# Kernel tuning notes

Measured on AMD Instinct MI355X. Metric: run time of the kernel, lower is better.

## Reference

```python
import jax, jax.numpy as jnp
import numpy as np

NEG = -10000.0
EPS = 1e-5

B, N, H, DEPTH = 4096, 64, 128, 3
H2 = H // 2


def setup_inputs() -> dict:
    key = jax.random.key(0)
    k1, k2, k3 = jax.random.split(key, 3)
    hidden_states = jax.random.normal(k1, (B, N, H), dtype=jnp.float32)
    li_vector_num = jax.random.randint(k2, (B,), 0, N + 1, dtype=jnp.int32)
    Ws = jax.random.normal(k3, (DEPTH, H, H2), dtype=jnp.float32) * (1.0 / np.sqrt(H))
    bs = jnp.zeros((DEPTH, H2), dtype=jnp.float32)
    ln_w = jnp.ones((DEPTH, H2), dtype=jnp.float32)
    ln_b = jnp.zeros((DEPTH, H2), dtype=jnp.float32)
    return {"hidden_states": hidden_states, "li_vector_num": li_vector_num,
            "Ws": Ws, "bs": bs, "ln_w": ln_w, "ln_b": ln_b}


def _subgraph(hidden_states, Ws, bs, ln_w, ln_b, li_vector_num):
    b, n, h = hidden_states.shape
    # padding mask: -10000 for invalid vectors (i >= li_vector_num), per polyline
    pad = jnp.where(jnp.arange(n)[None, :] >= li_vector_num[:, None], NEG, 0.0)
    pad = pad.astype(hidden_states.dtype)[:, :, None]  # [B,N,1]
    hs = hidden_states
    for l in range(Ws.shape[0]):
        # MLP: linear -> layernorm -> relu
        x = jnp.einsum('bnh,hk->bnk', hs, Ws[l]) + bs[l]
        mu = jnp.mean(x, axis=-1, keepdims=True)
        var = jnp.mean((x - mu) ** 2, axis=-1, keepdims=True)
        x = ln_w[l] * (x - mu) * jax.lax.rsqrt(var + EPS) + ln_b[l]
        enc = jax.nn.relu(x)  # [B,N,H2]
        m = enc + pad  # masked encoded states
        # leave-one-out max over vector dim via top-2 trick (replaces O(N^2) loop)
        top2 = jax.lax.top_k(jnp.swapaxes(m, 1, 2), 2)[0]  # [B,H2,2]
        top1b = top2[..., 0][:, None, :]  # [B,1,H2]
        top2b = top2[..., 1][:, None, :]  # [B,1,H2]
        loo = jnp.where(m == top1b, top2b, top1b)  # max over i != j
        loo = jnp.maximum(loo, m + NEG)            # faithful: j itself at -10000
        loo = jnp.maximum(loo, 0.0)                # torch.max(max_hidden, zeros)
        hs = jnp.concatenate([enc, loo], axis=-1)  # [B,N,H]
    return jnp.max(hs, axis=1)  # [B,H]


def reference(hidden_states, li_vector_num, Ws, bs, ln_w, ln_b):
    return _subgraph(hidden_states, Ws, bs, ln_w, ln_b, li_vector_num)
```

## Files before the change

### kernel.cpp

```cpp
#include <hip/hip_runtime.h>
#include <hip/hip_bf16.h>

#define NEGV (-10000.0f)
#define EPSV (1e-5f)
#define NINF (-3.4e38f)

typedef __attribute__((ext_vector_type(8))) short short8;
typedef __attribute__((ext_vector_type(4))) float floatx4;

constexpr int Bsz = 4096, Nv = 64, Hd = 128, DEPTH = 3, H2 = 64;
constexpr int HSTR = 136;

struct alignas(8) BH4 { __hip_bfloat162 a, b; };

__device__ __forceinline__ unsigned short f2b(float f) {
    unsigned int u = __builtin_bit_cast(unsigned int, f);
    u += 0x7fffu + ((u >> 16) & 1u);
    return (unsigned short)(u >> 16);
}

__device__ __forceinline__ void t2ins(float& t1, float& t2, float v) {
    float lo = fminf(t1, v); t1 = fmaxf(t1, v); t2 = fmaxf(t2, lo);
}
__device__ __forceinline__ void t2merge(float& t1, float& t2, float o1, float o2) {
    float lo = fminf(t1, o1); t1 = fmaxf(t1, o1); t2 = fmaxf(fmaxf(t2, o2), lo);
}

__global__ void prep_w(const float* __restrict__ Ws, unsigned short* __restrict__ wt) {
    int idx = blockIdx.x * 256 + threadIdx.x;
    if (idx < DEPTH * 8192) {
        int l = idx >> 13, o = idx & 8191;
        int j = o & 7, q = (o >> 3) & 63, hi = (o >> 9) & 3, kt = o >> 11;
        int k = kt * 32 + hi * 8 + j;
        int srccol = (q & 15) * 4 + (q >> 4);
        wt[idx] = f2b(Ws[l * 8192 + k * 64 + srccol]);
    }
}

__global__ __launch_bounds__(256, 4)
void subgraph_kernel(const float* __restrict__ hidden, const int* __restrict__ lvn,
                     const unsigned short* __restrict__ wt,
                     const float* __restrict__ bsv, const float* __restrict__ lnw,
                     const float* __restrict__ lnb, float* __restrict__ out)
{
    __shared__ __hip_bfloat16 hsb[Nv][HSTR];
    __shared__ float scbuf[4][128];

    const int b = blockIdx.x, t = threadIdx.x;
    const int L = lvn[b];
    const int lane = t & 63, wid = t >> 6;
    const int lr = lane & 15, hi = lane >> 4;
    const int arow = wid * 16 + lr;

    const float4* src = (const float4*)(hidden + (size_t)b * Nv * Hd);
#pragma unroll
    for (int i = 0; i < 8; ++i) {
        int idx4 = t + i * 256;
        float4 v = src[idx4];
        int flat = idx4 * 4, n = flat >> 7, h = flat & 127;
        BH4 pk;
        pk.a = __float22bfloat162_rn(make_float2(v.x, v.y));
        pk.b = __float22bfloat162_rn(make_float2(v.z, v.w));
        *(BH4*)&hsb[n][h] = pk;
    }

    float madd[4];
#pragma unroll
    for (int reg = 0; reg < 4; ++reg) {
        int row = wid * 16 + hi * 4 + reg;
        madd[reg] = (row >= L) ? NEGV : 0.0f;
    }
    __syncthreads();

    float encmax[4], loomax[4];

    for (int l = 0; l < DEPTH; ++l) {
        const unsigned short* wbase = wt + l * 8192;

        short8 af[4];
#pragma unroll
        for (int kt = 0; kt < 4; ++kt)
            af[kt] = *(const short8*)&hsb[arow][kt * 32 + hi * 8];

        floatx4 acc[4];
#pragma unroll
        for (int ct = 0; ct < 4; ++ct) { floatx4 z = {0.f, 0.f, 0.f, 0.f}; acc[ct] = z; }
#pragma unroll
        for (int kt = 0; kt < 4; ++kt)
#pragma unroll
            for (int ct = 0; ct < 4; ++ct) {
                short8 bf = *(const short8*)(wbase + ((kt * 4 + hi) * 64 + ct * 16 + lr) * 8);
                acc[ct] = __builtin_amdgcn_mfma_f32_16x16x32_bf16(af[kt], bf, acc[ct], 0, 0, 0);
            }

        float4 bias = *(const float4*)(bsv + l * H2 + 4 * lr);
        float4 gw   = *(const float4*)(lnw + l * H2 + 4 * lr);
        float4 gb   = *(const float4*)(lnb + l * H2 + 4 * lr);
        float enc[4][4];
#pragma unroll
        for (int reg = 0; reg < 4; ++reg) {
            float x0 = acc[0][reg] + bias.x;
            float x1 = acc[1][reg] + bias.y;
            float x2 = acc[2][reg] + bias.z;
            float x3 = acc[3][reg] + bias.w;
            float s = x0 + x1 + x2 + x3;
            float q = x0 * x0 + x1 * x1 + x2 * x2 + x3 * x3;
#pragma unroll
            for (int m = 1; m < 16; m <<= 1) {
                s += __shfl_xor(s, m, 64);
                q += __shfl_xor(q, m, 64);
            }
            float mu  = s * (1.0f / 64.0f);
            float var = fmaxf(q * (1.0f / 64.0f) - mu * mu, 0.0f);
            float rstd = rsqrtf(var + EPSV);
            enc[0][reg] = fmaxf(gw.x * (x0 - mu) * rstd + gb.x, 0.0f);
            enc[1][reg] = fmaxf(gw.y * (x1 - mu) * rstd + gb.y, 0.0f);
            enc[2][reg] = fmaxf(gw.z * (x2 - mu) * rstd + gb.z, 0.0f);
            enc[3][reg] = fmaxf(gw.w * (x3 - mu) * rstd + gb.w, 0.0f);
        }

        float t1[4], t2[4];
#pragma unroll
        for (int ct = 0; ct < 4; ++ct) {
            float a0 = enc[ct][0] + madd[0], a1 = enc[ct][1] + madd[1];
            float a2 = enc[ct][2] + madd[2], a3 = enc[ct][3] + madd[3];
            t1[ct] = fmaxf(a0, a1); t2[ct] = fminf(a0, a1);
            t2ins(t1[ct], t2[ct], a2);
            t2ins(t1[ct], t2[ct], a3);
            t2merge(t1[ct], t2[ct], __shfl_xor(t1[ct], 16, 64), __shfl_xor(t2[ct], 16, 64));
            t2merge(t1[ct], t2[ct], __shfl_xor(t1[ct], 32, 64), __shfl_xor(t2[ct], 32, 64));
        }
        if (hi == 0) {
#pragma unroll
            for (int ct = 0; ct < 4; ++ct)
                ((float2*)scbuf[wid])[ct * 16 + lr] = make_float2(t1[ct], t2[ct]);
        }
        __syncthreads();

        float f1[4], f2[4];
#pragma unroll
        for (int ct = 0; ct < 4; ++ct) { f1[ct] = NINF; f2[ct] = NINF; }
#pragma unroll
        for (int w = 0; w < 4; ++w)
#pragma unroll
            for (int ct = 0; ct < 4; ++ct) {
                float2 p = ((const float2*)scbuf[w])[ct * 16 + lr];
                t2merge(f1[ct], f2[ct], p.x, p.y);
            }

        if (l < DEPTH - 1) {
#pragma unroll
            for (int reg = 0; reg < 4; ++reg) {
                int row = wid * 16 + hi * 4 + reg;
                float lo[4];
#pragma unroll
                for (int ct = 0; ct < 4; ++ct) {
                    float mv = enc[ct][reg] + madd[reg];
                    float v = (mv == f1[ct]) ? f2[ct] : f1[ct];
                    v = fmaxf(v, mv + NEGV);
                    lo[ct] = fmaxf(v, 0.0f);
                }
                BH4 we, wl_;
                we.a  = __float22bfloat162_rn(make_float2(enc[0][reg], enc[1][reg]));
                we.b  = __float22bfloat162_rn(make_float2(enc[2][reg], enc[3][reg]));
                wl_.a = __float22bfloat162_rn(make_float2(lo[0], lo[1]));
                wl_.b = __float22bfloat162_rn(make_float2(lo[2], lo[3]));
                *(BH4*)&hsb[row][4 * lr]      = we;
                *(BH4*)&hsb[row][64 + 4 * lr] = wl_;
            }
            __syncthreads();
        } else {
#pragma unroll
            for (int ct = 0; ct < 4; ++ct) {
                float em = fmaxf(fmaxf(enc[ct][0], enc[ct][1]), fmaxf(enc[ct][2], enc[ct][3]));
                float lm = NINF;
#pragma unroll
                for (int reg = 0; reg < 4; ++reg) {
                    float mv = enc[ct][reg] + madd[reg];
                    float v = (mv == f1[ct]) ? f2[ct] : f1[ct];
                    v = fmaxf(v, mv + NEGV);
                    lm = fmaxf(lm, fmaxf(v, 0.0f));
                }
                em = fmaxf(em, __shfl_xor(em, 16, 64));
                em = fmaxf(em, __shfl_xor(em, 32, 64));
                lm = fmaxf(lm, __shfl_xor(lm, 16, 64));
                lm = fmaxf(lm, __shfl_xor(lm, 32, 64));
                encmax[ct] = em; loomax[ct] = lm;
            }
        }
    }

    __syncthreads();
    if (hi == 0) {
        float4 e = make_float4(encmax[0], encmax[1], encmax[2], encmax[3]);
        float4 o = make_float4(loomax[0], loomax[1], loomax[2], loomax[3]);
        *(float4*)&scbuf[wid][4 * lr]      = e;
        *(float4*)&scbuf[wid][64 + 4 * lr] = o;
    }
    __syncthreads();
    if (t < Hd) {
        float v = fmaxf(fmaxf(scbuf[0][t], scbuf[1][t]), fmaxf(scbuf[2][t], scbuf[3][t]));
        out[(size_t)b * Hd + t] = v;
    }
}

extern "C" void kernel_launch(void* const* d_in, const int* in_sizes, int n_in,
                              void* d_out, int out_size, void* d_ws, size_t ws_size,
                              hipStream_t stream) {
    const float* hidden = (const float*)d_in[0];
    const int*   lvn    = (const int*)d_in[1];
    const float* Ws     = (const float*)d_in[2];
    const float* bs     = (const float*)d_in[3];
    const float* lnwp   = (const float*)d_in[4];
    const float* lnbp   = (const float*)d_in[5];
    unsigned short* wt  = (unsigned short*)d_ws;
    float* outp = (float*)d_out;

    prep_w<<<(DEPTH * 8192 + 255) / 256, 256, 0, stream>>>(Ws, wt);
    subgraph_kernel<<<Bsz, 256, 0, stream>>>(hidden, lvn, wt, bs, lnwp, lnbp, outp);
}
```

Measured before the change: 68.98 us.

## Assign one polyline per wavefront, removing block barriers and LDS reductions

Each wavefront now processes a whole batch element (all 64 rows as four row tiles), so a block of four waves handles four polylines with a private LDS slab per wave. This drops all __syncthreads and the cross-wave top-2 and final max reductions through shared memory. Layer 0 loads fp32 inputs straight from global into MFMA A fragments instead of staging them in LDS, and each B fragment is reused across four row tiles. The cost is many more registers (64 accumulator floats plus 16 masks), hence launch bounds lowered to 2 blocks per SIMD, and a 4x larger LDS footprint per block, which may reduce occupancy.

```diff
diff --git a/kernel.cpp b/kernel.cpp
--- a/kernel.cpp
+++ b/kernel.cpp
@@ -37,150 +37,149 @@
     }
 }
 
-__global__ __launch_bounds__(256, 4)
+__global__ __launch_bounds__(256, 2)
 void subgraph_kernel(const float* __restrict__ hidden, const int* __restrict__ lvn,
                      const unsigned short* __restrict__ wt,
                      const float* __restrict__ bsv, const float* __restrict__ lnw,
                      const float* __restrict__ lnb, float* __restrict__ out)
 {
-    __shared__ __hip_bfloat16 hsb[Nv][HSTR];
-    __shared__ float scbuf[4][128];
-
-    const int b = blockIdx.x, t = threadIdx.x;
+    __shared__ __hip_bfloat16 hsw[4][Nv][HSTR];
+
+    const int t = threadIdx.x;
+    const int lane = t & 63, wid = t >> 6;
+    const int b = blockIdx.x * 4 + wid;
+    const int lr = lane & 15, hi = lane >> 4;
     const int L = lvn[b];
-    const int lane = t & 63, wid = t >> 6;
-    const int lr = lane & 15, hi = lane >> 4;
-    const int arow = wid * 16 + lr;
-
-    const float4* src = (const float4*)(hidden + (size_t)b * Nv * Hd);
-#pragma unroll
-    for (int i = 0; i < 8; ++i) {
-        int idx4 = t + i * 256;
-        float4 v = src[idx4];
-        int flat = idx4 * 4, n = flat >> 7, h = flat & 127;
-        BH4 pk;
-        pk.a = __float22bfloat162_rn(make_float2(v.x, v.y));
-        pk.b = __float22bfloat162_rn(make_float2(v.z, v.w));
-        *(BH4*)&hsb[n][h] = pk;
-    }
-
-    float madd[4];
-#pragma unroll
-    for (int reg = 0; reg < 4; ++reg) {
-        int row = wid * 16 + hi * 4 + reg;
-        madd[reg] = (row >= L) ? NEGV : 0.0f;
-    }
-    __syncthreads();
-
+
+    __hip_bfloat16 (*hs)[HSTR] = hsw[wid];
+
+    float madd[4][4];
+#pragma unroll
+    for (int rt = 0; rt < 4; ++rt)
+#pragma unroll
+        for (int reg = 0; reg < 4; ++reg)
+            madd[rt][reg] = ((rt * 16 + hi * 4 + reg) >= L) ? NEGV : 0.0f;
+
+    const float4* ab = (const float4*)(hidden + (size_t)b * Nv * Hd);
     float encmax[4], loomax[4];
 
+#pragma unroll
     for (int l = 0; l < DEPTH; ++l) {
-        const unsigned short* wbase = wt + l * 8192;
-
-        short8 af[4];
-#pragma unroll
-        for (int kt = 0; kt < 4; ++kt)
-            af[kt] = *(const short8*)&hsb[arow][kt * 32 + hi * 8];
-
-        floatx4 acc[4];
-#pragma unroll
-        for (int ct = 0; ct < 4; ++ct) { floatx4 z = {0.f, 0.f, 0.f, 0.f}; acc[ct] = z; }
-#pragma unroll
-        for (int kt = 0; kt < 4; ++kt)
+        const short8* wfrag = (const short8*)(wt + l * 8192);
+
+        floatx4 acc[4][4];
+#pragma unroll
+        for (int rt = 0; rt < 4; ++rt)
+#pragma unroll
+            for (int ct = 0; ct < 4; ++ct) { floatx4 z = {0.f,0.f,0.f,0.f}; acc[rt][ct] = z; }
+
+#pragma unroll
+        for (int kt = 0; kt < 4; ++kt) {
+            short8 af[4];
+            if (l == 0) {
+#pragma unroll
+                for (int rt = 0; rt < 4; ++rt) {
+                    int fi = (rt * 16 + lr) * 32 + kt * 8 + hi * 2;
+                    float4 f0 = ab[fi], f1 = ab[fi + 1];
+                    union { short8 s; __hip_bfloat162 h[4]; } u;
+                    u.h[0] = __float22bfloat162_rn(make_float2(f0.x, f0.y));
+                    u.h[1] = __float22bfloat162_rn(make_float2(f0.z, f0.w));
+                    u.h[2] = __float22bfloat162_rn(make_float2(f1.x, f1.y));
+                    u.h[3] = __float22bfloat162_rn(make_float2(f1.z, f1.w));
+                    af[rt] = u.s;
+                }
+            } else {
+#pragma unroll
+                for (int rt = 0; rt < 4; ++rt)
+                    af[rt] = *(const short8*)&hs[rt * 16 + lr][kt * 32 + hi * 8];
+            }
 #pragma unroll
             for (int ct = 0; ct < 4; ++ct) {
-                short8 bf = *(const short8*)(wbase + ((kt * 4 + hi) * 64 + ct * 16 + lr) * 8);
-                acc[ct] = __builtin_amdgcn_mfma_f32_16x16x32_bf16(af[kt], bf, acc[ct], 0, 0, 0);
-            }
+                short8 bf = wfrag[(kt * 4 + hi) * 64 + ct * 16 + lr];
+#pragma unroll
+                for (int rt = 0; rt < 4; ++rt)
+                    acc[rt][ct] = __builtin_amdgcn_mfma_f32_16x16x32_bf16(af[rt], bf, acc[rt][ct], 0, 0, 0);
+            }
+        }
 
         float4 bias = *(const float4*)(bsv + l * H2 + 4 * lr);
         float4 gw   = *(const float4*)(lnw + l * H2 + 4 * lr);
         float4 gb   = *(const float4*)(lnb + l * H2 + 4 * lr);
-        float enc[4][4];
-#pragma unroll
-        for (int reg = 0; reg < 4; ++reg) {
-            float x0 = acc[0][reg] + bias.x;
-            float x1 = acc[1][reg] + bias.y;
-            float x2 = acc[2][reg] + bias.z;
-            float x3 = acc[3][reg] + bias.w;
-            float s = x0 + x1 + x2 + x3;
-            float q = x0 * x0 + x1 * x1 + x2 * x2 + x3 * x3;
-#pragma unroll
-            for (int m = 1; m < 16; m <<= 1) {
-                s += __shfl_xor(s, m, 64);
-                q += __shfl_xor(q, m, 64);
-            }
-            float mu  = s * (1.0f / 64.0f);
-            float var = fmaxf(q * (1.0f / 64.0f) - mu * mu, 0.0f);
-            float rstd = rsqrtf(var + EPSV);
-            enc[0][reg] = fmaxf(gw.x * (x0 - mu) * rstd + gb.x, 0.0f);
-            enc[1][reg] = fmaxf(gw.y * (x1 - mu) * rstd + gb.y, 0.0f);
-            enc[2][reg] = fmaxf(gw.z * (x2 - mu) * rstd + gb.z, 0.0f);
-            enc[3][reg] = fmaxf(gw.w * (x3 - mu) * rstd + gb.w, 0.0f);
+#pragma unroll
+        for (int rt = 0; rt < 4; ++rt)
+#pragma unroll
+            for (int reg = 0; reg < 4; ++reg) {
+                float x0 = acc[rt][0][reg] + bias.x;
+                float x1 = acc[rt][1][reg] + bias.y;
+                float x2 = acc[rt][2][reg] + bias.z;
+                float x3 = acc[rt][3][reg] + bias.w;
+                float s = x0 + x1 + x2 + x3;
+                float q = x0 * x0 + x1 * x1 + x2 * x2 + x3 * x3;
+#pragma unroll
+                for (int m = 1; m < 16; m <<= 1) {
+                    s += __shfl_xor(s, m, 64);
+                    q += __shfl_xor(q, m, 64);
+                }
+                float mu  = s * (1.0f / 64.0f);
+                float var = fmaxf(q * (1.0f / 64.0f) - mu * mu, 0.0f);
+                float rstd = rsqrtf(var + EPSV);
+                acc[rt][0][reg] = fmaxf(gw.x * (x0 - mu) * rstd + gb.x, 0.0f);
+                acc[rt][1][reg] = fmaxf(gw.y * (x1 - mu) * rstd + gb.y, 0.0f);
+                acc[rt][2][reg] = fmaxf(gw.z * (x2 - mu) * rstd + gb.z, 0.0f);
+                acc[rt][3][reg] = fmaxf(gw.w * (x3 - mu) * rstd + gb.w, 0.0f);
+            }
+
+        float f1v[4], f2v[4];
+#pragma unroll
+        for (int ct = 0; ct < 4; ++ct) {
+            float t1 = NINF, t2 = NINF;
+#pragma unroll
+            for (int rt = 0; rt < 4; ++rt)
+#pragma unroll
+                for (int reg = 0; reg < 4; ++reg)
+                    t2ins(t1, t2, acc[rt][ct][reg] + madd[rt][reg]);
+            t2merge(t1, t2, __shfl_xor(t1, 16, 64), __shfl_xor(t2, 16, 64));
+            t2merge(t1, t2, __shfl_xor(t1, 32, 64), __shfl_xor(t2, 32, 64));
+            f1v[ct] = t1; f2v[ct] = t2;
         }
 
-        float t1[4], t2[4];
-#pragma unroll
-        for (int ct = 0; ct < 4; ++ct) {
-            float a0 = enc[ct][0] + madd[0], a1 = enc[ct][1] + madd[1];
-            float a2 = enc[ct][2] + madd[2], a3 = enc[ct][3] + madd[3];
-            t1[ct] = fmaxf(a0, a1); t2[ct] = fminf(a0, a1);
-            t2ins(t1[ct], t2[ct], a2);
-            t2ins(t1[ct], t2[ct], a3);
-            t2merge(t1[ct], t2[ct], __shfl_xor(t1[ct], 16, 64), __shfl_xor(t2[ct], 16, 64));
-            t2merge(t1[ct], t2[ct], __shfl_xor(t1[ct], 32, 64), __shfl_xor(t2[ct], 32, 64));
-        }
-        if (hi == 0) {
-#pragma unroll
-            for (int ct = 0; ct < 4; ++ct)
-                ((float2*)scbuf[wid])[ct * 16 + lr] = make_float2(t1[ct], t2[ct]);
-        }
-        __syncthreads();
-
-        float f1[4], f2[4];
-#pragma unroll
-        for (int ct = 0; ct < 4; ++ct) { f1[ct] = NINF; f2[ct] = NINF; }
-#pragma unroll
-        for (int w = 0; w < 4; ++w)
+        if (l < DEPTH - 1) {
+#pragma unroll
+            for (int rt = 0; rt < 4; ++rt)
+#pragma unroll
+                for (int reg = 0; reg < 4; ++reg) {
+                    int row = rt * 16 + hi * 4 + reg;
+                    float lo[4];
+#pragma unroll
+                    for (int ct = 0; ct < 4; ++ct) {
+                        float mv = acc[rt][ct][reg] + madd[rt][reg];
+                        float v = (mv == f1v[ct]) ? f2v[ct] : f1v[ct];
+                        v = fmaxf(v, mv + NEGV);
+                        lo[ct] = fmaxf(v, 0.0f);
+                    }
+                    BH4 we, wl_;
+                    we.a  = __float22bfloat162_rn(make_float2(acc[rt][0][reg], acc[rt][1][reg]));
+                    we.b  = __float22bfloat162_rn(make_float2(acc[rt][2][reg], acc[rt][3][reg]));
+                    wl_.a = __float22bfloat162_rn(make_float2(lo[0], lo[1]));
+                    wl_.b = __float22bfloat162_rn(make_float2(lo[2], lo[3]));
+                    *(BH4*)&hs[row][4 * lr]      = we;
+                    *(BH4*)&hs[row][64 + 4 * lr] = wl_;
+                }
+        } else {
 #pragma unroll
             for (int ct = 0; ct < 4; ++ct) {
-                float2 p = ((const float2*)scbuf[w])[ct * 16 + lr];
-                t2merge(f1[ct], f2[ct], p.x, p.y);
-            }
-
-        if (l < DEPTH - 1) {
-#pragma unroll
-            for (int reg = 0; reg < 4; ++reg) {
-                int row = wid * 16 + hi * 4 + reg;
-                float lo[4];
-#pragma unroll
-                for (int ct = 0; ct < 4; ++ct) {
-                    float mv = enc[ct][reg] + madd[reg];
-                    float v = (mv == f1[ct]) ? f2[ct] : f1[ct];
-                    v = fmaxf(v, mv + NEGV);
-                    lo[ct] = fmaxf(v, 0.0f);
-                }
-                BH4 we, wl_;
-                we.a  = __float22bfloat162_rn(make_float2(enc[0][reg], enc[1][reg]));
-                we.b  = __float22bfloat162_rn(make_float2(enc[2][reg], enc[3][reg]));
-                wl_.a = __float22bfloat162_rn(make_float2(lo[0], lo[1]));
-                wl_.b = __float22bfloat162_rn(make_float2(lo[2], lo[3]));
-                *(BH4*)&hsb[row][4 * lr]      = we;
-                *(BH4*)&hsb[row][64 + 4 * lr] = wl_;
-            }
-            __syncthreads();
-        } else {
-#pragma unroll
-            for (int ct = 0; ct < 4; ++ct) {
-                float em = fmaxf(fmaxf(enc[ct][0], enc[ct][1]), fmaxf(enc[ct][2], enc[ct][3]));
-                float lm = NINF;
-#pragma unroll
-                for (int reg = 0; reg < 4; ++reg) {
-                    float mv = enc[ct][reg] + madd[reg];
-                    float v = (mv == f1[ct]) ? f2[ct] : f1[ct];
-                    v = fmaxf(v, mv + NEGV);
-                    lm = fmaxf(lm, fmaxf(v, 0.0f));
-                }
+                float em = NINF, lm = NINF;
+#pragma unroll
+                for (int rt = 0; rt < 4; ++rt)
+#pragma unroll
+                    for (int reg = 0; reg < 4; ++reg) {
+                        float e = acc[rt][ct][reg];
+                        em = fmaxf(em, e);
+                        float mv = e + madd[rt][reg];
+                        float v = (mv == f1v[ct]) ? f2v[ct] : f1v[ct];
+                        v = fmaxf(v, mv + NEGV);
+                        lm = fmaxf(lm, fmaxf(v, 0.0f));
+                    }
                 em = fmaxf(em, __shfl_xor(em, 16, 64));
                 em = fmaxf(em, __shfl_xor(em, 32, 64));
                 lm = fmaxf(lm, __shfl_xor(lm, 16, 64));
@@ -190,17 +189,11 @@
         }
     }
 
-    __syncthreads();
     if (hi == 0) {
         float4 e = make_float4(encmax[0], encmax[1], encmax[2], encmax[3]);
         float4 o = make_float4(loomax[0], loomax[1], loomax[2], loomax[3]);
-        *(float4*)&scbuf[wid][4 * lr]      = e;
-        *(float4*)&scbuf[wid][64 + 4 * lr] = o;
-    }
-    __syncthreads();
-    if (t < Hd) {
-        float v = fmaxf(fmaxf(scbuf[0][t], scbuf[1][t]), fmaxf(scbuf[2][t], scbuf[3][t]));
-        out[(size_t)b * Hd + t] = v;
+        *(float4*)(out + (size_t)b * Hd + 4 * lr)      = e;
+        *(float4*)(out + (size_t)b * Hd + 64 + 4 * lr) = o;
     }
 }
 
@@ -217,5 +210,5 @@
     float* outp = (float*)d_out;
 
     prep_w<<<(DEPTH * 8192 + 255) / 256, 256, 0, stream>>>(Ws, wt);
-    subgraph_kernel<<<Bsz, 256, 0, stream>>>(hidden, lvn, wt, bs, lnwp, lnbp, outp);
-}
+    subgraph_kernel<<<Bsz / 4, 256, 0, stream>>>(hidden, lvn, wt, bs, lnwp, lnbp, outp);
+}
```

Measured after the change: 68.26 us. No clear change (-1.0%).
